# Kernel optimization log

Hardware: AMD Instinct MI355X
Metric: run time of the kernel (lower is better)

The kernel has to match this reference:

```python
import jax, jax.numpy as jnp
import numpy as np
from jax import lax

STRIDE = 16
SCALE = 16.0
ANCHOR_DIMS = (1.0, 2.0, 4.0, 8.0, 16.0, 32.0)
PRE_NMS_TOP_N = 6000
POST_NMS_TOP_N = 300
NMS_THRESH = 0.7


def conv2d(x, w, b, pad):
    y = lax.conv_general_dilated(x, w, (1, 1), [(pad, pad), (pad, pad)],
                                 dimension_numbers=("NCHW", "OIHW", "NCHW"))
    return y + b[None, :, None, None]


def setup_inputs() -> dict:
    key = jax.random.key(0)
    ks = jax.random.split(key, 6)
    B, C, H, W = 1, 1024, 128, 128
    A = len(ANCHOR_DIMS)
    return {
        "base_features": jax.random.normal(ks[0], (B, C, H, W), jnp.float32),
        "image_metadata": jnp.array([[H * STRIDE, W * STRIDE, 1.0]], jnp.float32),
        "gt_boxes": jax.random.uniform(ks[1], (B, 20, 5), jnp.float32) * 100.0,
        "W_conv": jax.random.normal(ks[2], (512, C, 3, 3), jnp.float32) / np.sqrt(C * 9.0),
        "b_conv": jnp.zeros((512,), jnp.float32),
        "W_cls": jax.random.normal(ks[3], (A, 512, 1, 1), jnp.float32) / np.sqrt(512.0),
        "b_cls": jnp.zeros((A,), jnp.float32),
        "W_bbox": jax.random.normal(ks[4], (4 * A, 512, 1, 1), jnp.float32) * 0.01,
        "b_bbox": jnp.zeros((4 * A,), jnp.float32),
    }


def _make_anchors(H, W):
    # square anchors of size dim*scale, centered on each feature cell
    dims = jnp.asarray(ANCHOR_DIMS, jnp.float32) * SCALE          # [A]
    cy = (jnp.arange(H, dtype=jnp.float32) + 0.5) * STRIDE        # [H]
    cx = (jnp.arange(W, dtype=jnp.float32) + 0.5) * STRIDE        # [W]
    half = 0.5 * dims[None, None, :]                              # [1,1,A]
    CX = cx[None, :, None]
    CY = cy[:, None, None]
    anchors = jnp.stack(jnp.broadcast_arrays(CX - half, CY - half, CX + half, CY + half), axis=-1)
    return anchors.reshape(-1, 4)                                 # [(H*W*A),4], order (h,w,a)


def _nms_fixed(boxes, scores):
    # boxes [N,4] already sorted by score desc; greedy NMS, POST_NMS_TOP_N picks
    x1, y1, x2, y2 = boxes[:, 0], boxes[:, 1], boxes[:, 2], boxes[:, 3]
    areas = jnp.maximum(x2 - x1, 0.0) * jnp.maximum(y2 - y1, 0.0)

    def body(i, state):
        alive, keep = state
        masked = jnp.where(alive, scores, -jnp.inf)
        j = jnp.argmax(masked)
        valid = masked[j] > -jnp.inf
        keep = keep.at[i].set(jnp.where(valid, j, -1).astype(jnp.int32))
        bj = boxes[j]
        iw = jnp.maximum(jnp.minimum(x2, bj[2]) - jnp.maximum(x1, bj[0]), 0.0)
        ih = jnp.maximum(jnp.minimum(y2, bj[3]) - jnp.maximum(y1, bj[1]), 0.0)
        inter = iw * ih
        iou = inter / (areas + areas[j] - inter + 1e-9)
        alive = alive & (iou <= NMS_THRESH)
        return alive, keep

    alive0 = jnp.ones(boxes.shape[0], bool)
    keep0 = jnp.full((POST_NMS_TOP_N,), -1, jnp.int32)
    _, keep = lax.fori_loop(0, POST_NMS_TOP_N, body, (alive0, keep0))
    return keep


def _proposal(prob, bbox, image_metadata):
    # original layer operates on detached tensors (.data)
    prob = lax.stop_gradient(prob)
    bbox = lax.stop_gradient(bbox)
    B, A, H, W = prob.shape
    anchors = _make_anchors(H, W)                                 # [N,4]
    scores = prob[0].transpose(1, 2, 0).reshape(-1)               # (h,w,a)
    deltas = bbox[0].reshape(A, 4, H, W).transpose(2, 3, 0, 1).reshape(-1, 4)
    wa = anchors[:, 2] - anchors[:, 0]
    ha = anchors[:, 3] - anchors[:, 1]
    cxa = anchors[:, 0] + 0.5 * wa
    cya = anchors[:, 1] + 0.5 * ha
    pcx = deltas[:, 0] * wa + cxa
    pcy = deltas[:, 1] * ha + cya
    pw = jnp.exp(deltas[:, 2]) * wa
    ph = jnp.exp(deltas[:, 3]) * ha
    boxes = jnp.stack([pcx - 0.5 * pw, pcy - 0.5 * ph, pcx + 0.5 * pw, pcy + 0.5 * ph], axis=1)
    im_h, im_w = image_metadata[0, 0], image_metadata[0, 1]
    boxes = jnp.stack([
        jnp.clip(boxes[:, 0], 0.0, im_w), jnp.clip(boxes[:, 1], 0.0, im_h),
        jnp.clip(boxes[:, 2], 0.0, im_w), jnp.clip(boxes[:, 3], 0.0, im_h)], axis=1)
    top_scores, top_idx = lax.top_k(scores, PRE_NMS_TOP_N)
    top_boxes = boxes[top_idx]
    keep = _nms_fixed(top_boxes, top_scores)
    sel = jnp.where(keep >= 0, keep, 0)
    kept = top_boxes[sel] * (keep >= 0).astype(top_boxes.dtype)[:, None]
    rois = jnp.concatenate([jnp.zeros((POST_NMS_TOP_N, 1), top_boxes.dtype), kept], axis=1)
    return rois                                                   # [POST_NMS_TOP_N, 5]


def reference(base_features, image_metadata, gt_boxes, W_conv, b_conv, W_cls, b_cls, W_bbox, b_bbox):
    conv1 = jax.nn.relu(conv2d(base_features, W_conv, b_conv, pad=1))   # [B,512,H,W]
    score = conv2d(conv1, W_cls, b_cls, pad=0)                          # [B,A,H,W]
    B, A, H, W = score.shape
    s2 = score.reshape(B, 2, (A * H) // 2, W)                           # RPN.reshape(x, 2)
    prob = jax.nn.softmax(s2, axis=1).reshape(B, A, H, W)               # reshape back to A channels
    bbox = conv2d(conv1, W_bbox, b_bbox, pad=0)                         # [B,4A,H,W]
    rois = _proposal(prob, bbox, image_metadata)
    return rois, prob, bbox
```

## Files before the change

kernel.cpp:

```cpp
#include <hip/hip_runtime.h>
#include <math.h>

typedef unsigned int u32;
typedef unsigned long long u64;
typedef short s16x8 __attribute__((ext_vector_type(8)));
typedef float f32x4 __attribute__((ext_vector_type(4)));

#define HH 128
#define WW 128
#define NPIX (128*128)
#define NANCH (NPIX*6)
#define KPRE 6000
#define KPOST 300
#define SORT_CAP 16384
#define RW 96
#define NMS_T 0.7f

#define OUT_PROB 1500
#define OUT_BBOX (1500 + 98304)

#define WS_CONV1 ((size_t)0)
#define WS_XTH   ((size_t)33554432)
#define WS_WPH   ((size_t)100663296)
#define WS_BOXES ((size_t)33554432)
#define WS_SCORE (WS_BOXES + 1572864)
#define WS_KEYS  (WS_SCORE + 393216)
#define WS_TB    (WS_KEYS + 131072)
#define WS_AREA  (WS_TB + 98304)
#define WS_SUP   (WS_AREA + 24576)
#define WS_HIST  (WS_SUP + 4718592)
#define WS_CTRL  (WS_HIST + 262144)
#define WS_KEEP  (WS_CTRL + 256)
#define WS_SKEYS (WS_KEEP + 1280)

__device__ __forceinline__ unsigned short f2bf(float x) {
    u32 b = __float_as_uint(x);
    u32 r = (b + 0x7FFFu + ((b >> 16) & 1u)) >> 16;
    return (unsigned short)r;
}

__device__ __forceinline__ void gl_lds16(const void* g, void* l) {
    __builtin_amdgcn_global_load_lds(
        (__attribute__((address_space(1))) const void*)g,
        (__attribute__((address_space(3))) void*)l,
        16, 0, 0);
}

__global__ void k_init(u32* __restrict__ hist, u32* __restrict__ ctrl,
                       int* __restrict__ keep, u64* __restrict__ keys) {
    int t = blockIdx.x * blockDim.x + threadIdx.x;
    if (t < 65536) hist[t] = 0u;
    if (t < 64)    ctrl[t] = 0u;
    if (t < 304)   keep[t] = -1;
    if (t < SORT_CAP) keys[t] = ~0ULL;
}

__global__ __launch_bounds__(256) void k_xsplit(const float* __restrict__ in,
                                                unsigned short* __restrict__ xth) {
    unsigned short* xtl = xth + 16777216;
    __shared__ unsigned short Th[64][72];
    __shared__ unsigned short Tl[64][72];
    const int px0 = blockIdx.x * 64;
    const int c0  = blockIdx.y * 64;
    const int t = threadIdx.x;
    const int r = t >> 4;
    const int p4 = (t & 15) * 4;
#pragma unroll
    for (int i = 0; i < 4; ++i) {
        int cr = r + 16 * i;
        float4 v = *(const float4*)(in + (size_t)(c0 + cr) * NPIX + px0 + p4);
        float vv[4] = {v.x, v.y, v.z, v.w};
#pragma unroll
        for (int k = 0; k < 4; ++k) {
            unsigned short h = f2bf(vv[k]);
            float hf = __uint_as_float((u32)h << 16);
            unsigned short l = f2bf(vv[k] - hf);
            Th[p4 + k][cr] = h;
            Tl[p4 + k][cr] = l;
        }
    }
    __syncthreads();
    const int p = t >> 2, q = t & 3;
    unsigned short* dh = xth + (size_t)(px0 + p) * 1024 + c0 + q * 16;
    unsigned short* dl = xtl + (size_t)(px0 + p) * 1024 + c0 + q * 16;
    *(uint4*)dh       = *(const uint4*)&Th[p][q * 16];
    *(uint4*)(dh + 8) = *(const uint4*)&Th[p][q * 16 + 8];
    *(uint4*)dl       = *(const uint4*)&Tl[p][q * 16];
    *(uint4*)(dl + 8) = *(const uint4*)&Tl[p][q * 16 + 8];
}

__global__ __launch_bounds__(256) void k_wpack(const float* __restrict__ w,
                                               unsigned short* __restrict__ wph,
                                               float* __restrict__ zstash) {
    if (blockIdx.x == 0 && threadIdx.x < 128) zstash[threadIdx.x] = 0.f;
    int id = blockIdx.x * 256 + threadIdx.x;
    int oc = id >> 10, c = id & 1023;
    const float* src = w + (size_t)oc * 9216 + c * 9;
#pragma unroll
    for (int tap = 0; tap < 9; ++tap) {
        float x = src[tap];
        unsigned short h = f2bf(x);
        unsigned short l = f2bf(x - __uint_as_float((u32)h << 16));
        wph[(size_t)tap * 524288 + id] = h;
        wph[4718592 + (size_t)tap * 524288 + id] = l;
    }
}

__global__ __launch_bounds__(256, 2) void k_conv3m(const unsigned short* __restrict__ xt,
                                                   const unsigned short* __restrict__ wp,
                                                   const float* __restrict__ bias,
                                                   const unsigned short* __restrict__ zst,
                                                   float* __restrict__ out) {
    const int ocg = blockIdx.x;
    const int y   = blockIdx.y;
    const int oc0 = ocg * 128;
    const int tid = threadIdx.x;
    const int lane = tid & 63;
    const int w    = tid >> 6;
    const int l15  = lane & 15;
    const int quad = lane >> 4;
    const int hoc  = w >> 1, hpx = w & 1;

    __shared__ __align__(16) unsigned short Lds[32768];

    const int lg  = lane & 3;
    const int lr  = lane >> 2;

    const unsigned short* xsrc[4];
    int xstep[4];
    const unsigned short* wsrc[4];

    int wp_pl[4], wp_ocr[4], wp_gs[4];
#pragma unroll
    for (int j = 0; j < 4; ++j) {
        int i = w + 4 * j;
        wp_pl[j]  = i >> 3;
        wp_ocr[j] = (i & 7) * 16 + lr;
        wp_gs[j]  = lg ^ ((wp_ocr[j] >> 1) & 3);
    }
    int xp_pl[4], xp_p[4], xp_gs[4];
#pragma unroll
    for (int j = 0; j < 4; ++j) {
        int i = w + 4 * j;
        xp_pl[j] = i >> 3;
        xp_p[j]  = (i & 7) * 16 + lr;
        xp_gs[j] = lg ^ ((xp_p[j] >> 1) & 3);
    }

    auto set_tap = [&](int tap) {
        int dy = tap / 3, dx = tap - dy * 3;
        int yy = y + dy - 1;
        bool yok = (yy >= 0) && (yy < HH);
#pragma unroll
        for (int j = 0; j < 4; ++j) {
            int x = dx - 1 + xp_p[j];
            bool ok = yok && (x >= 0) && (x < WW);
            xsrc[j] = ok ? xt + (size_t)xp_pl[j] * 16777216
                              + (size_t)(yy * WW + x) * 1024 + xp_gs[j] * 8
                         : zst + lg * 8;
            xstep[j] = ok ? 32 : 0;
        }
#pragma unroll
        for (int j = 0; j < 4; ++j)
            wsrc[j] = wp + (size_t)wp_pl[j] * 4718592 + (size_t)tap * 524288
                        + (size_t)(oc0 + wp_ocr[j]) * 1024 + wp_gs[j] * 8;
    };

    auto issue = [&](int sel) {
        const int bo = sel * 16384;
#pragma unroll
        for (int j = 0; j < 4; ++j) {
            gl_lds16(xsrc[j], &Lds[bo + (w + 4 * j) * 512]);
            xsrc[j] += xstep[j];
        }
#pragma unroll
        for (int j = 0; j < 4; ++j) {
            gl_lds16(wsrc[j], &Lds[bo + 8192 + (w + 4 * j) * 512]);
            wsrc[j] += 32;
        }
    };

    const int g  = quad ^ ((l15 >> 1) & 3);
    const int bB0 = (hpx * 64 + l15) * 32 + g * 8;
    const int bA0 = 8192 + (hoc * 64 + l15) * 32 + g * 8;

    f32x4 acc[4][4];
#pragma unroll
    for (int og = 0; og < 4; ++og)
#pragma unroll
        for (int nt = 0; nt < 4; ++nt) acc[og][nt] = (f32x4){0.f, 0.f, 0.f, 0.f};

    set_tap(0);
    issue(0);

    for (int s = 0; s < 288; ++s) {
        const int cur = s & 1;
        __syncthreads();
        if (s + 1 < 288) {
            int s1 = s + 1;
            if ((s1 & 31) == 0) set_tap(s1 >> 5);
            issue(s1 & 1);
        }

        const int bo = cur * 16384;
        s16x8 ah[4], al[4];
#pragma unroll
        for (int og = 0; og < 4; ++og) {
            ah[og] = *(const s16x8*)&Lds[bo + bA0 + og * 512];
            al[og] = *(const s16x8*)&Lds[bo + bA0 + 4096 + og * 512];
        }
#pragma unroll
        for (int nt = 0; nt < 4; ++nt) {
            const s16x8 bh = *(const s16x8*)&Lds[bo + bB0 + nt * 512];
            const s16x8 bl = *(const s16x8*)&Lds[bo + bB0 + 4096 + nt * 512];
#pragma unroll
            for (int og = 0; og < 4; ++og) {
                acc[og][nt] = __builtin_amdgcn_mfma_f32_16x16x32_bf16(ah[og], bh, acc[og][nt], 0, 0, 0);
                acc[og][nt] = __builtin_amdgcn_mfma_f32_16x16x32_bf16(ah[og], bl, acc[og][nt], 0, 0, 0);
                acc[og][nt] = __builtin_amdgcn_mfma_f32_16x16x32_bf16(al[og], bh, acc[og][nt], 0, 0, 0);
            }
        }
    }

#pragma unroll
    for (int og = 0; og < 4; ++og) {
#pragma unroll
        for (int nt = 0; nt < 4; ++nt) {
#pragma unroll
            for (int rg = 0; rg < 4; ++rg) {
                const int oc = oc0 + hoc * 64 + og * 16 + quad * 4 + rg;
                const int px = hpx * 64 + nt * 16 + l15;
                float v = acc[og][nt][rg] + bias[oc];
                out[(size_t)oc * NPIX + y * WW + px] = fmaxf(v, 0.f);
            }
        }
    }
}

__global__ __launch_bounds__(256) void k_conv1(const float* __restrict__ conv1,
                                               const float* __restrict__ wcls,
                                               const float* __restrict__ bcls,
                                               const float* __restrict__ wbox,
                                               const float* __restrict__ bboxb,
                                               float* __restrict__ out) {
    const int tid = threadIdx.x;
    const int og = tid >> 4, pg = tid & 15;
    const int px0 = blockIdx.x * 64;
    __shared__ __align__(16) float Wl[32][32];
    __shared__ __align__(16) float Xl[32][64];
    __shared__ float Sc[6][64];

    float a0[4] = {0, 0, 0, 0}, a1[4] = {0, 0, 0, 0};

    for (int cc = 0; cc < 16; ++cc) {
        {
            int u = tid;
            int row = (u * 4) >> 5;
            int col = (u * 4) & 31;
            float4 v;
            if (row < 6)       v = *(const float4*)(wcls + row * 512 + cc * 32 + col);
            else if (row < 30) v = *(const float4*)(wbox + (row - 6) * 512 + cc * 32 + col);
            else               v = make_float4(0.f, 0.f, 0.f, 0.f);
            *(float4*)&Wl[row][col] = v;
        }
        for (int u = tid; u < 512; u += 256) {
            int row = (u * 4) >> 6, col = (u * 4) & 63;
            *(float4*)&Xl[row][col] =
                *(const float4*)(conv1 + (size_t)(cc * 32 + row) * NPIX + px0 + col);
        }
        __syncthreads();
#pragma unroll
        for (int cp = 0; cp < 32; ++cp) {
            const float4 x = *(const float4*)&Xl[cp][pg * 4];
            const float w0 = Wl[og][cp];
            const float w1 = Wl[og + 16][cp];
            a0[0] = fmaf(w0, x.x, a0[0]); a0[1] = fmaf(w0, x.y, a0[1]);
            a0[2] = fmaf(w0, x.z, a0[2]); a0[3] = fmaf(w0, x.w, a0[3]);
            a1[0] = fmaf(w1, x.x, a1[0]); a1[1] = fmaf(w1, x.y, a1[1]);
            a1[2] = fmaf(w1, x.z, a1[2]); a1[3] = fmaf(w1, x.w, a1[3]);
        }
        __syncthreads();
    }
    const int pxb = px0 + pg * 4;
    if (og < 6) {
        const float bc = bcls[og];
#pragma unroll
        for (int kk = 0; kk < 4; ++kk) Sc[og][pg * 4 + kk] = a0[kk] + bc;
    } else {
        const float bb = bboxb[og - 6];
#pragma unroll
        for (int kk = 0; kk < 4; ++kk)
            out[OUT_BBOX + (size_t)(og - 6) * NPIX + pxb + kk] = a0[kk] + bb;
    }
    if (og + 16 < 30) {
        const float bb = bboxb[og + 10];
#pragma unroll
        for (int kk = 0; kk < 4; ++kk)
            out[OUT_BBOX + (size_t)(og + 10) * NPIX + pxb + kk] = a1[kk] + bb;
    }
    __syncthreads();
    if (og < 6) {
        const int pa = og < 3 ? og + 3 : og - 3;
#pragma unroll
        for (int kk = 0; kk < 4; ++kk) {
            const float s = Sc[og][pg * 4 + kk], sp = Sc[pa][pg * 4 + kk];
            out[OUT_PROB + (size_t)og * NPIX + pxb + kk] = 1.0f / (1.0f + expf(sp - s));
        }
    }
}

__global__ void k_decode(const float* __restrict__ out, const float* __restrict__ meta,
                         float4* __restrict__ boxes, float* __restrict__ scores) {
#pragma clang fp contract(off)
    int t = blockIdx.x * blockDim.x + threadIdx.x;
    if (t >= NANCH) return;
    int a = t >> 14;
    int pix = t & 16383;
    int yc = pix >> 7, xc = pix & 127;
    int n = pix * 6 + a;
    float sc = out[OUT_PROB + (size_t)a * NPIX + pix];
    float d0 = out[OUT_BBOX + (size_t)(a * 4 + 0) * NPIX + pix];
    float d1 = out[OUT_BBOX + (size_t)(a * 4 + 1) * NPIX + pix];
    float d2 = out[OUT_BBOX + (size_t)(a * 4 + 2) * NPIX + pix];
    float d3 = out[OUT_BBOX + (size_t)(a * 4 + 3) * NPIX + pix];
    const float dims = (float)(16 << a);
    const float cxa = (xc + 0.5f) * 16.f;
    const float cya = (yc + 0.5f) * 16.f;
    float pcx = d0 * dims + cxa;
    float pcy = d1 * dims + cya;
    float pw  = expf(d2) * dims;
    float ph  = expf(d3) * dims;
    float imh = meta[0], imw = meta[1];
    float x1 = fminf(fmaxf(pcx - 0.5f * pw, 0.f), imw);
    float y1 = fminf(fmaxf(pcy - 0.5f * ph, 0.f), imh);
    float x2 = fminf(fmaxf(pcx + 0.5f * pw, 0.f), imw);
    float y2 = fminf(fmaxf(pcy + 0.5f * ph, 0.f), imh);
    boxes[n] = make_float4(x1, y1, x2, y2);
    scores[n] = sc;
}

__global__ void k_hist(const float* __restrict__ scores, u32* __restrict__ hist) {
    int t = blockIdx.x * blockDim.x + threadIdx.x;
    if (t >= NANCH) return;
    u32 b = __float_as_uint(scores[t]) >> 16;
    atomicAdd(&hist[b], 1u);
}

__global__ void k_select(const u32* __restrict__ hist, u32* __restrict__ ctrl) {
    __shared__ u32 S[256];
    __shared__ u32 U[256];
    const int tid = threadIdx.x;
    u32 s = 0;
    for (int i = 0; i < 256; ++i) s += hist[tid * 256 + i];
    S[tid] = s;
    __syncthreads();
    if (tid == 0) {
        u32 acc = 0;
        for (int t2 = 255; t2 >= 0; --t2) { U[t2] = acc; acc += S[t2]; }
    }
    __syncthreads();
    if (U[tid] < KPRE && U[tid] + S[tid] >= KPRE) {
        u32 acc = U[tid];
        for (int b = tid * 256 + 255; b >= tid * 256; --b) {
            u32 h = hist[b];
            if (acc + h >= KPRE) { ctrl[1] = (u32)b; ctrl[2] = acc; break; }
            acc += h;
        }
    }
}

__global__ void k_compact(const float* __restrict__ scores, u32* __restrict__ ctrl,
                          u64* __restrict__ keys) {
    int t = blockIdx.x * blockDim.x + threadIdx.x;
    if (t >= NANCH) return;
    u32 bits = __float_as_uint(scores[t]);
    if ((bits >> 16) >= ctrl[1]) {
        u32 pos = atomicAdd(&ctrl[0], 1u);
        if (pos < SORT_CAP) keys[pos] = ((u64)(~bits) << 32) | (u32)t;
    }
}

__global__ __launch_bounds__(1024) void k_sort_local(u64* __restrict__ keys) {
    __shared__ u64 lds[8192];
    const int tid = threadIdx.x;
    u64* g = keys + blockIdx.x * 8192;
    for (int u = tid; u < 8192; u += 1024) lds[u] = g[u];
    __syncthreads();
    for (int k = 2; k <= 8192; k <<= 1) {
        for (int j = k >> 1; j > 0; j >>= 1) {
            for (int u = tid; u < 4096; u += 1024) {
                int i = ((u & ~(j - 1)) << 1) | (u & (j - 1));
                int l = i | j;
                bool up = (i & k) == 0;
                u64 x = lds[i], y2 = lds[l];
                if ((x > y2) == up) { lds[i] = y2; lds[l] = x; }
            }
            __syncthreads();
        }
    }
    for (int u = tid; u < 8192; u += 1024) g[u] = lds[u];
}

__global__ void k_merge(const u64* __restrict__ keys, u64* __restrict__ skeys) {
    int i = blockIdx.x * blockDim.x + threadIdx.x;
    if (i >= KPRE) return;
    const u64* A = keys;
    const u64* B = keys + 8192;
    int lo = i > 8192 ? i - 8192 : 0;
    int hi = i < 8192 ? i : 8192;
    while (lo < hi) {
        int a = (lo + hi) >> 1;
        if (A[a] < B[i - a - 1]) lo = a + 1; else hi = a;
    }
    int a = lo, b = i - lo;
    u64 va = (a < 8192) ? A[a] : ~0ULL;
    u64 vb = (b < 8192) ? B[b] : ~0ULL;
    skeys[i] = va < vb ? va : vb;
}

__global__ void k_gather(const u64* __restrict__ skeys, const float4* __restrict__ boxes,
                         float4* __restrict__ tb, float* __restrict__ areas) {
#pragma clang fp contract(off)
    int i = blockIdx.x * blockDim.x + threadIdx.x;
    if (i >= KPRE) return;
    u32 n = (u32)(skeys[i] & 0xFFFFFFFFULL);
    float4 b = boxes[n];
    tb[i] = b;
    areas[i] = fmaxf(b.z - b.x, 0.f) * fmaxf(b.w - b.y, 0.f);
}

__global__ __launch_bounds__(256) void k_bitmap(const float4* __restrict__ tb,
                                                const float* __restrict__ areas,
                                                u64* __restrict__ suppr) {
#pragma clang fp contract(off)
    const int i = blockIdx.x;
    const int lane = threadIdx.x & 63;
    const int wv = threadIdx.x >> 6;
    const float4 bi = tb[i];
    const float ai = areas[i];
    for (int Wd = wv; Wd < RW; Wd += 4) {
        int j = Wd * 64 + lane;
        bool sup = false;
        if (j < KPRE) {
            float4 bj = tb[j];
            float iw = fmaxf(fminf(bi.z, bj.z) - fmaxf(bi.x, bj.x), 0.f);
            float ih = fmaxf(fminf(bi.w, bj.w) - fmaxf(bi.y, bj.y), 0.f);
            float inter = iw * ih;
            float denom = ((areas[j] + ai) - inter) + 1e-9f;
            sup = (inter / denom) > NMS_T;
        }
        u64 m = __ballot(sup);
        if (lane == 0) suppr[(size_t)i * RW + Wd] = m;
    }
}

__global__ void k_scan(const u64* __restrict__ suppr, int* __restrict__ keep) {
    const int lane = threadIdx.x;
    u64 a0 = (lane < 93) ? ~0ULL : (lane == 93 ? ((1ULL << 48) - 1) : 0ULL);
    const int w1 = lane + 64;
    u64 a1 = (w1 < 93) ? ~0ULL : (w1 == 93 ? ((1ULL << 48) - 1) : 0ULL);
    int kept = 0;
    int i = 0;
    while (kept < KPOST) {
        int wi = i >> 6;
        if (wi >= 94) break;
        u64 wvv = (wi < 64) ? __shfl(a0, wi) : __shfl(a1, wi - 64);
        wvv &= (~0ULL) << (i & 63);
        if (wvv == 0ULL) { i = (wi + 1) << 6; continue; }
        int b = __ffsll((long long)wvv) - 1;
        i = (wi << 6) + b;
        if (lane == 0) keep[kept] = i;
        kept++;
        const u64* row = suppr + (size_t)i * RW;
        u64 s0 = row[lane];
        u64 s1 = (lane + 64 < RW) ? row[lane + 64] : 0ULL;
        a0 &= ~s0;
        a1 &= ~s1;
        i++;
    }
}

__global__ void k_rois(const int* __restrict__ keep, const float4* __restrict__ tb,
                       float* __restrict__ out) {
    int r = blockIdx.x * blockDim.x + threadIdx.x;
    if (r >= KPOST) return;
    int k = keep[r];
    float4 b = make_float4(0.f, 0.f, 0.f, 0.f);
    if (k >= 0) b = tb[k];
    out[r * 5 + 0] = 0.f;
    out[r * 5 + 1] = b.x;
    out[r * 5 + 2] = b.y;
    out[r * 5 + 3] = b.z;
    out[r * 5 + 4] = b.w;
}

extern "C" void kernel_launch(void* const* d_in, const int* in_sizes, int n_in,
                              void* d_out, int out_size, void* d_ws, size_t ws_size,
                              hipStream_t stream) {
    (void)in_sizes; (void)n_in; (void)out_size; (void)ws_size;
    const float* x     = (const float*)d_in[0];
    const float* meta  = (const float*)d_in[1];
    const float* wc3   = (const float*)d_in[3];
    const float* bc3   = (const float*)d_in[4];
    const float* wcls  = (const float*)d_in[5];
    const float* bcls  = (const float*)d_in[6];
    const float* wbox  = (const float*)d_in[7];
    const float* bboxb = (const float*)d_in[8];
    float* out = (float*)d_out;
    char* ws = (char*)d_ws;

    float*  conv1  = (float*)(ws + WS_CONV1);
    float4* boxes  = (float4*)(ws + WS_BOXES);
    float*  scores = (float*)(ws + WS_SCORE);
    u64*    keys   = (u64*)(ws + WS_KEYS);
    float4* tb     = (float4*)(ws + WS_TB);
    float*  areas  = (float*)(ws + WS_AREA);
    u64*    suppr  = (u64*)(ws + WS_SUP);
    u32*    hist   = (u32*)(ws + WS_HIST);
    u32*    ctrl   = (u32*)(ws + WS_CTRL);
    int*    keep   = (int*)(ws + WS_KEEP);
    u64*    skeys  = (u64*)(ws + WS_SKEYS);

    float* zstash = out;

    unsigned short* xth = (unsigned short*)(ws + WS_XTH);
    unsigned short* wph = (unsigned short*)(ws + WS_WPH);
    k_xsplit<<<dim3(256, 16), 256, 0, stream>>>(x, xth);
    k_wpack<<<2048, 256, 0, stream>>>(wc3, wph, zstash);
    k_conv3m<<<dim3(4, 128), 256, 0, stream>>>(xth, wph, bc3,
                                               (const unsigned short*)zstash, conv1);

    k_init<<<256, 256, 0, stream>>>(hist, ctrl, keep, keys);
    k_conv1<<<256, 256, 0, stream>>>(conv1, wcls, bcls, wbox, bboxb, out);
    k_decode<<<384, 256, 0, stream>>>(out, meta, boxes, scores);
    k_hist<<<384, 256, 0, stream>>>(scores, hist);
    k_select<<<1, 256, 0, stream>>>(hist, ctrl);
    k_compact<<<384, 256, 0, stream>>>(scores, ctrl, keys);
    k_sort_local<<<2, 1024, 0, stream>>>(keys);
    k_merge<<<24, 256, 0, stream>>>(keys, skeys);
    k_gather<<<24, 256, 0, stream>>>(skeys, boxes, tb, areas);
    k_bitmap<<<6000, 256, 0, stream>>>(tb, areas, suppr);
    k_scan<<<1, 64, 0, stream>>>(suppr, keep);
    k_rois<<<2, 256, 0, stream>>>(keep, tb, out);
}
```

Baseline: 936.8 us.

## Prepack conv weights into MFMA fragment layout and use 32x32x16 bf16 MFMA

Repacks the 3x3 conv weights on the device into per-lane fragment records so each wave loads its A operands straight from global memory into registers, double-buffered across stages, instead of staging them through LDS. Switches the inner product from 16x16x32 to 32x32x16 bf16 MFMA with a 2x2 tile of 16-wide accumulators, and halves LDS use to the activation tile only. This removes LDS traffic and bank pressure for weights and raises the math done per fragment load. In exchange it adds register pressure from the prefetched weight fragments, and the global weight loads are no longer shared across waves through LDS.

Result: slower. 989.5 us (+5.6%).

```diff
diff --git a/kernel.cpp b/kernel.cpp
--- a/kernel.cpp
+++ b/kernel.cpp
@@ -5,6 +5,7 @@
 typedef unsigned long long u64;
 typedef short s16x8 __attribute__((ext_vector_type(8)));
 typedef float f32x4 __attribute__((ext_vector_type(4)));
+typedef float f32x16 __attribute__((ext_vector_type(16)));
 
 #define HH 128
 #define WW 128
@@ -96,13 +97,25 @@
     int id = blockIdx.x * 256 + threadIdx.x;
     int oc = id >> 10, c = id & 1023;
     const float* src = w + (size_t)oc * 9216 + c * 9;
+    const int ocg  = oc >> 7;
+    const int hoc  = (oc >> 6) & 1;
+    const int og   = (oc >> 5) & 1;
+    const int l31  = oc & 31;
+    const int cblk = c >> 5;
+    const int ks   = (c >> 4) & 1;
+    const int lhi  = (c >> 3) & 1;
+    const int e    = c & 7;
+    const int lane = lhi * 32 + l31;
+    const size_t rec0 = ((size_t)cblk * 4 + ocg) * 2 + hoc;
+    const size_t off0 = (size_t)(og * 2 + ks) * 512 + lane * 8 + e;
 #pragma unroll
     for (int tap = 0; tap < 9; ++tap) {
         float x = src[tap];
         unsigned short h = f2bf(x);
         unsigned short l = f2bf(x - __uint_as_float((u32)h << 16));
-        wph[(size_t)tap * 524288 + id] = h;
-        wph[4718592 + (size_t)tap * 524288 + id] = l;
+        size_t rec = rec0 + (size_t)tap * 256;
+        wph[rec * 4096 + off0]        = h;
+        wph[rec * 4096 + 2048 + off0] = l;
     }
 }
 
@@ -117,27 +130,18 @@
     const int tid = threadIdx.x;
     const int lane = tid & 63;
     const int w    = tid >> 6;
-    const int l15  = lane & 15;
-    const int quad = lane >> 4;
+    const int l31  = lane & 31;
+    const int lhi  = lane >> 5;
     const int hoc  = w >> 1, hpx = w & 1;
-
-    __shared__ __align__(16) unsigned short Lds[32768];
+    const int wrec = ocg * 2 + hoc;
+
+    __shared__ __align__(16) unsigned short Lds[16384];
 
     const int lg  = lane & 3;
     const int lr  = lane >> 2;
 
     const unsigned short* xsrc[4];
     int xstep[4];
-    const unsigned short* wsrc[4];
-
-    int wp_pl[4], wp_ocr[4], wp_gs[4];
-#pragma unroll
-    for (int j = 0; j < 4; ++j) {
-        int i = w + 4 * j;
-        wp_pl[j]  = i >> 3;
-        wp_ocr[j] = (i & 7) * 16 + lr;
-        wp_gs[j]  = lg ^ ((wp_ocr[j] >> 1) & 3);
-    }
     int xp_pl[4], xp_p[4], xp_gs[4];
 #pragma unroll
     for (int j = 0; j < 4; ++j) {
@@ -160,77 +164,107 @@
                          : zst + lg * 8;
             xstep[j] = ok ? 32 : 0;
         }
-#pragma unroll
-        for (int j = 0; j < 4; ++j)
-            wsrc[j] = wp + (size_t)wp_pl[j] * 4718592 + (size_t)tap * 524288
-                        + (size_t)(oc0 + wp_ocr[j]) * 1024 + wp_gs[j] * 8;
     };
 
     auto issue = [&](int sel) {
-        const int bo = sel * 16384;
+        const int bo = sel * 8192;
 #pragma unroll
         for (int j = 0; j < 4; ++j) {
             gl_lds16(xsrc[j], &Lds[bo + (w + 4 * j) * 512]);
             xsrc[j] += xstep[j];
         }
-#pragma unroll
-        for (int j = 0; j < 4; ++j) {
-            gl_lds16(wsrc[j], &Lds[bo + 8192 + (w + 4 * j) * 512]);
-            wsrc[j] += 32;
-        }
     };
 
-    const int g  = quad ^ ((l15 >> 1) & 3);
-    const int bB0 = (hpx * 64 + l15) * 32 + g * 8;
-    const int bA0 = 8192 + (hoc * 64 + l15) * 32 + g * 8;
-
-    f32x4 acc[4][4];
-#pragma unroll
-    for (int og = 0; og < 4; ++og)
-#pragma unroll
-        for (int nt = 0; nt < 4; ++nt) acc[og][nt] = (f32x4){0.f, 0.f, 0.f, 0.f};
+    int xoff[2][2];
+#pragma unroll
+    for (int nt = 0; nt < 2; ++nt)
+#pragma unroll
+        for (int ks = 0; ks < 2; ++ks) {
+            int px = hpx * 64 + nt * 32 + l31;
+            int gk = ks * 2 + lhi;
+            xoff[nt][ks] = px * 32 + ((gk ^ ((px >> 1) & 3)) * 8);
+        }
+
+    f32x16 acc[2][2];
+#pragma unroll
+    for (int og = 0; og < 2; ++og)
+#pragma unroll
+        for (int nt = 0; nt < 2; ++nt)
+#pragma unroll
+            for (int r = 0; r < 16; ++r) acc[og][nt][r] = 0.f;
+
+    s16x8 wA[8], wB[8];
 
     set_tap(0);
     issue(0);
-
-    for (int s = 0; s < 288; ++s) {
-        const int cur = s & 1;
-        __syncthreads();
-        if (s + 1 < 288) {
-            int s1 = s + 1;
-            if ((s1 & 31) == 0) set_tap(s1 >> 5);
-            issue(s1 & 1);
-        }
-
-        const int bo = cur * 16384;
-        s16x8 ah[4], al[4];
-#pragma unroll
-        for (int og = 0; og < 4; ++og) {
-            ah[og] = *(const s16x8*)&Lds[bo + bA0 + og * 512];
-            al[og] = *(const s16x8*)&Lds[bo + bA0 + 4096 + og * 512];
-        }
-#pragma unroll
-        for (int nt = 0; nt < 4; ++nt) {
-            const s16x8 bh = *(const s16x8*)&Lds[bo + bB0 + nt * 512];
-            const s16x8 bl = *(const s16x8*)&Lds[bo + bB0 + 4096 + nt * 512];
-#pragma unroll
-            for (int og = 0; og < 4; ++og) {
-                acc[og][nt] = __builtin_amdgcn_mfma_f32_16x16x32_bf16(ah[og], bh, acc[og][nt], 0, 0, 0);
-                acc[og][nt] = __builtin_amdgcn_mfma_f32_16x16x32_bf16(ah[og], bl, acc[og][nt], 0, 0, 0);
-                acc[og][nt] = __builtin_amdgcn_mfma_f32_16x16x32_bf16(al[og], bh, acc[og][nt], 0, 0, 0);
-            }
-        }
-    }
-
-#pragma unroll
-    for (int og = 0; og < 4; ++og) {
-#pragma unroll
-        for (int nt = 0; nt < 4; ++nt) {
-#pragma unroll
-            for (int rg = 0; rg < 4; ++rg) {
-                const int oc = oc0 + hoc * 64 + og * 16 + quad * 4 + rg;
-                const int px = hpx * 64 + nt * 16 + l15;
-                float v = acc[og][nt][rg] + bias[oc];
+    {
+        const s16x8* p = (const s16x8*)wp + (size_t)wrec * 512 + lane;
+#pragma unroll
+        for (int f = 0; f < 8; ++f) wA[f] = p[f * 64];
+    }
+
+#define STAGE(S, CUR, WC, WN)                                                   \
+    {                                                                           \
+        __syncthreads();                                                        \
+        if ((S) + 1 < 288) {                                                    \
+            if ((((S) + 1) & 31) == 0) set_tap(((S) + 1) >> 5);                 \
+            issue(((S) + 1) & 1);                                               \
+        }                                                                       \
+        {                                                                       \
+            int sn = ((S) + 1 < 288) ? (S) + 1 : 0;                             \
+            const s16x8* p = (const s16x8*)wp +                                 \
+                             ((size_t)sn * 8 + wrec) * 512 + lane;              \
+            _Pragma("unroll")                                                   \
+            for (int f = 0; f < 8; ++f) WN[f] = p[f * 64];                      \
+        }                                                                       \
+        const int bo = (CUR) * 8192;                                            \
+        s16x8 xh[2][2], xl[2][2];                                               \
+        _Pragma("unroll")                                                       \
+        for (int nt = 0; nt < 2; ++nt)                                          \
+            _Pragma("unroll")                                                   \
+            for (int ks = 0; ks < 2; ++ks) {                                    \
+                xh[nt][ks] = *(const s16x8*)&Lds[bo + xoff[nt][ks]];            \
+                xl[nt][ks] = *(const s16x8*)&Lds[bo + xoff[nt][ks] + 4096];     \
+            }                                                                   \
+        _Pragma("unroll")                                                       \
+        for (int ks = 0; ks < 2; ++ks) {                                        \
+            _Pragma("unroll")                                                   \
+            for (int og = 0; og < 2; ++og)                                      \
+                _Pragma("unroll")                                               \
+                for (int nt = 0; nt < 2; ++nt)                                  \
+                    acc[og][nt] = __builtin_amdgcn_mfma_f32_32x32x16_bf16(      \
+                        WC[og * 2 + ks], xh[nt][ks], acc[og][nt], 0, 0, 0);     \
+            _Pragma("unroll")                                                   \
+            for (int og = 0; og < 2; ++og)                                      \
+                _Pragma("unroll")                                               \
+                for (int nt = 0; nt < 2; ++nt)                                  \
+                    acc[og][nt] = __builtin_amdgcn_mfma_f32_32x32x16_bf16(      \
+                        WC[og * 2 + ks], xl[nt][ks], acc[og][nt], 0, 0, 0);     \
+            _Pragma("unroll")                                                   \
+            for (int og = 0; og < 2; ++og)                                      \
+                _Pragma("unroll")                                               \
+                for (int nt = 0; nt < 2; ++nt)                                  \
+                    acc[og][nt] = __builtin_amdgcn_mfma_f32_32x32x16_bf16(      \
+                        WC[4 + og * 2 + ks], xh[nt][ks], acc[og][nt], 0, 0, 0); \
+        }                                                                       \
+    }
+
+    for (int s = 0; s < 288; s += 2) {
+        STAGE(s, 0, wA, wB)
+        STAGE(s + 1, 1, wB, wA)
+    }
+#undef STAGE
+
+#pragma unroll
+    for (int og = 0; og < 2; ++og) {
+#pragma unroll
+        for (int nt = 0; nt < 2; ++nt) {
+            const int px = hpx * 64 + nt * 32 + l31;
+#pragma unroll
+            for (int r = 0; r < 16; ++r) {
+                const int row = (r & 3) + 8 * (r >> 2) + 4 * lhi;
+                const int oc = oc0 + hoc * 64 + og * 32 + row;
+                float v = acc[og][nt][r] + bias[oc];
                 out[(size_t)oc * NPIX + y * WW + px] = fmaxf(v, 0.f);
             }
         }
```

## Stream conv weights directly to registers and deepen activation LDS pipeline to four stages

Applied to the files above, without the earlier changes.

Repacks the split-bf16 conv weights into a per-wave, fragment-ordered layout, so each wave loads its A operands straight from global memory into registers with register double-buffering instead of staging them through LDS. The freed LDS is used for a four-buffer activation ring with three stages in flight. The per-stage full barrier wait is replaced by a partial vmcnt wait plus a raw barrier. This aims to cut LDS traffic and barrier stalls in the main 3x3 conv GEMM. The cost is more register pressure and more global weight reads per wave, since the weight tile is no longer shared through LDS.

Measured after the change: 986.9 us. 1.05x slower.

```diff
diff --git a/kernel.cpp b/kernel.cpp
--- a/kernel.cpp
+++ b/kernel.cpp
@@ -96,13 +96,25 @@
     int id = blockIdx.x * 256 + threadIdx.x;
     int oc = id >> 10, c = id & 1023;
     const float* src = w + (size_t)oc * 9216 + c * 9;
+    const int ocg  = oc >> 7;
+    const int hoc  = (oc >> 6) & 1;
+    const int og   = (oc >> 4) & 3;
+    const int l15  = oc & 15;
+    const int cblk = c >> 5;
+    const int q    = (c >> 3) & 3;
+    const int e    = c & 7;
+    const int lane = q * 16 + l15;
+    const size_t rec0 = ((size_t)cblk * 4 + ocg) * 2 + hoc;
+    const size_t offh = (size_t)(og * 2 + 0) * 512 + lane * 8 + e;
+    const size_t offl = (size_t)(og * 2 + 1) * 512 + lane * 8 + e;
 #pragma unroll
     for (int tap = 0; tap < 9; ++tap) {
         float x = src[tap];
         unsigned short h = f2bf(x);
         unsigned short l = f2bf(x - __uint_as_float((u32)h << 16));
-        wph[(size_t)tap * 524288 + id] = h;
-        wph[4718592 + (size_t)tap * 524288 + id] = l;
+        size_t rec = rec0 + (size_t)tap * 256;
+        wph[rec * 4096 + offh] = h;
+        wph[rec * 4096 + offl] = l;
     }
 }
 
@@ -120,6 +132,7 @@
     const int l15  = lane & 15;
     const int quad = lane >> 4;
     const int hoc  = w >> 1, hpx = w & 1;
+    const int wrec = ocg * 2 + hoc;
 
     __shared__ __align__(16) unsigned short Lds[32768];
 
@@ -128,16 +141,6 @@
 
     const unsigned short* xsrc[4];
     int xstep[4];
-    const unsigned short* wsrc[4];
-
-    int wp_pl[4], wp_ocr[4], wp_gs[4];
-#pragma unroll
-    for (int j = 0; j < 4; ++j) {
-        int i = w + 4 * j;
-        wp_pl[j]  = i >> 3;
-        wp_ocr[j] = (i & 7) * 16 + lr;
-        wp_gs[j]  = lg ^ ((wp_ocr[j] >> 1) & 3);
-    }
     int xp_pl[4], xp_p[4], xp_gs[4];
 #pragma unroll
     for (int j = 0; j < 4; ++j) {
@@ -147,10 +150,10 @@
         xp_gs[j] = lg ^ ((xp_p[j] >> 1) & 3);
     }
 
-    auto set_tap = [&](int tap) {
+    auto set_tap = [&](int tap, bool dead) {
         int dy = tap / 3, dx = tap - dy * 3;
         int yy = y + dy - 1;
-        bool yok = (yy >= 0) && (yy < HH);
+        bool yok = !dead && (yy >= 0) && (yy < HH);
 #pragma unroll
         for (int j = 0; j < 4; ++j) {
             int x = dx - 1 + xp_p[j];
@@ -160,29 +163,19 @@
                          : zst + lg * 8;
             xstep[j] = ok ? 32 : 0;
         }
-#pragma unroll
-        for (int j = 0; j < 4; ++j)
-            wsrc[j] = wp + (size_t)wp_pl[j] * 4718592 + (size_t)tap * 524288
-                        + (size_t)(oc0 + wp_ocr[j]) * 1024 + wp_gs[j] * 8;
     };
 
-    auto issue = [&](int sel) {
-        const int bo = sel * 16384;
+    auto issue = [&](int buf) {
+        const int bo = buf * 8192;
 #pragma unroll
         for (int j = 0; j < 4; ++j) {
             gl_lds16(xsrc[j], &Lds[bo + (w + 4 * j) * 512]);
             xsrc[j] += xstep[j];
         }
-#pragma unroll
-        for (int j = 0; j < 4; ++j) {
-            gl_lds16(wsrc[j], &Lds[bo + 8192 + (w + 4 * j) * 512]);
-            wsrc[j] += 32;
-        }
     };
 
-    const int g  = quad ^ ((l15 >> 1) & 3);
+    const int g   = quad ^ ((l15 >> 1) & 3);
     const int bB0 = (hpx * 64 + l15) * 32 + g * 8;
-    const int bA0 = 8192 + (hoc * 64 + l15) * 32 + g * 8;
 
     f32x4 acc[4][4];
 #pragma unroll
@@ -190,37 +183,63 @@
 #pragma unroll
         for (int nt = 0; nt < 4; ++nt) acc[og][nt] = (f32x4){0.f, 0.f, 0.f, 0.f};
 
-    set_tap(0);
+    s16x8 wA[8], wB[8];
+
+    set_tap(0, false);
     issue(0);
-
-    for (int s = 0; s < 288; ++s) {
-        const int cur = s & 1;
-        __syncthreads();
-        if (s + 1 < 288) {
-            int s1 = s + 1;
-            if ((s1 & 31) == 0) set_tap(s1 >> 5);
-            issue(s1 & 1);
-        }
-
-        const int bo = cur * 16384;
-        s16x8 ah[4], al[4];
-#pragma unroll
-        for (int og = 0; og < 4; ++og) {
-            ah[og] = *(const s16x8*)&Lds[bo + bA0 + og * 512];
-            al[og] = *(const s16x8*)&Lds[bo + bA0 + 4096 + og * 512];
-        }
-#pragma unroll
-        for (int nt = 0; nt < 4; ++nt) {
-            const s16x8 bh = *(const s16x8*)&Lds[bo + bB0 + nt * 512];
-            const s16x8 bl = *(const s16x8*)&Lds[bo + bB0 + 4096 + nt * 512];
-#pragma unroll
-            for (int og = 0; og < 4; ++og) {
-                acc[og][nt] = __builtin_amdgcn_mfma_f32_16x16x32_bf16(ah[og], bh, acc[og][nt], 0, 0, 0);
-                acc[og][nt] = __builtin_amdgcn_mfma_f32_16x16x32_bf16(ah[og], bl, acc[og][nt], 0, 0, 0);
-                acc[og][nt] = __builtin_amdgcn_mfma_f32_16x16x32_bf16(al[og], bh, acc[og][nt], 0, 0, 0);
-            }
-        }
-    }
+    {
+        const s16x8* p = (const s16x8*)wp + (size_t)wrec * 512 + lane;
+#pragma unroll
+        for (int f = 0; f < 8; ++f) wA[f] = p[f * 64];
+    }
+    issue(1);
+    issue(2);
+
+#define STAGE(S, WC, WN)                                                        \
+    {                                                                           \
+        asm volatile("s_waitcnt vmcnt(16)" ::: "memory");                       \
+        __builtin_amdgcn_s_barrier();                                           \
+        {                              \
+            int sn = ((S) + 1 < 288) ? (S) + 1 : 0;                             \
+            const s16x8* p = (const s16x8*)wp +                                 \
+                             ((size_t)sn * 8 + wrec) * 512 + lane;              \
+            _Pragma("unroll")                                                   \
+            for (int f = 0; f < 8; ++f) WN[f] = p[f * 64];                      \
+        }                                                                       \
+        {               \
+            int s3 = (S) + 3;                                                   \
+            if ((s3 & 31) == 0) set_tap(s3 >> 5, s3 >= 288);                    \
+            issue(s3 & 3);                                                      \
+        }                                                                       \
+        const int bo = ((S) & 3) * 8192;                                        \
+        s16x8 bh[4], bl[4];                                                     \
+        _Pragma("unroll")                                                       \
+        for (int nt = 0; nt < 4; ++nt) {                                        \
+            bh[nt] = *(const s16x8*)&Lds[bo + bB0 + nt * 512];                  \
+            bl[nt] = *(const s16x8*)&Lds[bo + bB0 + 4096 + nt * 512];           \
+        }                                                                       \
+        _Pragma("unroll")                                                       \
+        for (int nt = 0; nt < 4; ++nt) {                                        \
+            _Pragma("unroll")                                                   \
+            for (int og = 0; og < 4; ++og)                                      \
+                acc[og][nt] = __builtin_amdgcn_mfma_f32_16x16x32_bf16(          \
+                    WC[og * 2], bh[nt], acc[og][nt], 0, 0, 0);                  \
+            _Pragma("unroll")                                                   \
+            for (int og = 0; og < 4; ++og)                                      \
+                acc[og][nt] = __builtin_amdgcn_mfma_f32_16x16x32_bf16(          \
+                    WC[og * 2], bl[nt], acc[og][nt], 0, 0, 0);                  \
+            _Pragma("unroll")                                                   \
+            for (int og = 0; og < 4; ++og)                                      \
+                acc[og][nt] = __builtin_amdgcn_mfma_f32_16x16x32_bf16(          \
+                    WC[og * 2 + 1], bh[nt], acc[og][nt], 0, 0, 0);              \
+        }                                                                       \
+    }
+
+    for (int s = 0; s < 288; s += 2) {
+        STAGE(s, wA, wB)
+        STAGE(s + 1, wB, wA)
+    }
+#undef STAGE
 
 #pragma unroll
     for (int og = 0; og < 4; ++og) {
```

## Replace bitmap NMS with single-block greedy NMS and fuse small post-processing kernels

Applied to the files above, without the earlier changes.

Drops the full 6000x6000 suppression-bitmap kernel and serial scan. They are replaced by one 1024-thread block that keeps all candidate boxes in registers and runs greedy NMS directly: a block-wide min finds the next alive box, then every thread suppresses its own boxes against it. The histogram atomic is folded into decode, and merge is fused with gather and rois, which removes several launches and the 4.7MB bitmap traffic. The cost is up to 300 serial iterations, each with three block barriers, on a single CU.

New measurement: 1.259 ms. 1.34x slower.

```diff
diff --git a/kernel.cpp b/kernel.cpp
--- a/kernel.cpp
+++ b/kernel.cpp
@@ -13,7 +13,6 @@
 #define KPRE 6000
 #define KPOST 300
 #define SORT_CAP 16384
-#define RW 96
 #define NMS_T 0.7f
 
 #define OUT_PROB 1500
@@ -27,11 +26,8 @@
 #define WS_KEYS  (WS_SCORE + 393216)
 #define WS_TB    (WS_KEYS + 131072)
 #define WS_AREA  (WS_TB + 98304)
-#define WS_SUP   (WS_AREA + 24576)
-#define WS_HIST  (WS_SUP + 4718592)
+#define WS_HIST  (WS_AREA + 24576)
 #define WS_CTRL  (WS_HIST + 262144)
-#define WS_KEEP  (WS_CTRL + 256)
-#define WS_SKEYS (WS_KEEP + 1280)
 
 __device__ __forceinline__ unsigned short f2bf(float x) {
     u32 b = __float_as_uint(x);
@@ -47,11 +43,10 @@
 }
 
 __global__ void k_init(u32* __restrict__ hist, u32* __restrict__ ctrl,
-                       int* __restrict__ keep, u64* __restrict__ keys) {
+                       u64* __restrict__ keys) {
     int t = blockIdx.x * blockDim.x + threadIdx.x;
     if (t < 65536) hist[t] = 0u;
     if (t < 64)    ctrl[t] = 0u;
-    if (t < 304)   keep[t] = -1;
     if (t < SORT_CAP) keys[t] = ~0ULL;
 }
 
@@ -310,7 +305,8 @@
 }
 
 __global__ void k_decode(const float* __restrict__ out, const float* __restrict__ meta,
-                         float4* __restrict__ boxes, float* __restrict__ scores) {
+                         float4* __restrict__ boxes, float* __restrict__ scores,
+                         u32* __restrict__ hist) {
 #pragma clang fp contract(off)
     int t = blockIdx.x * blockDim.x + threadIdx.x;
     if (t >= NANCH) return;
@@ -337,13 +333,7 @@
     float y2 = fminf(fmaxf(pcy + 0.5f * ph, 0.f), imh);
     boxes[n] = make_float4(x1, y1, x2, y2);
     scores[n] = sc;
-}
-
-__global__ void k_hist(const float* __restrict__ scores, u32* __restrict__ hist) {
-    int t = blockIdx.x * blockDim.x + threadIdx.x;
-    if (t >= NANCH) return;
-    u32 b = __float_as_uint(scores[t]) >> 16;
-    atomicAdd(&hist[b], 1u);
+    atomicAdd(&hist[__float_as_uint(sc) >> 16], 1u);
 }
 
 __global__ void k_select(const u32* __restrict__ hist, u32* __restrict__ ctrl) {
@@ -401,7 +391,10 @@
     for (int u = tid; u < 8192; u += 1024) g[u] = lds[u];
 }
 
-__global__ void k_merge(const u64* __restrict__ keys, u64* __restrict__ skeys) {
+__global__ void k_mergegather(const u64* __restrict__ keys,
+                              const float4* __restrict__ boxes,
+                              float4* __restrict__ tb, float* __restrict__ areas) {
+#pragma clang fp contract(off)
     int i = blockIdx.x * blockDim.x + threadIdx.x;
     if (i >= KPRE) return;
     const u64* A = keys;
@@ -415,83 +408,82 @@
     int a = lo, b = i - lo;
     u64 va = (a < 8192) ? A[a] : ~0ULL;
     u64 vb = (b < 8192) ? B[b] : ~0ULL;
-    skeys[i] = va < vb ? va : vb;
-}
-
-__global__ void k_gather(const u64* __restrict__ skeys, const float4* __restrict__ boxes,
-                         float4* __restrict__ tb, float* __restrict__ areas) {
+    u64 v = va < vb ? va : vb;
+    u32 n = (u32)(v & 0xFFFFFFFFULL);
+    float4 bx = boxes[n];
+    tb[i] = bx;
+    areas[i] = fmaxf(bx.z - bx.x, 0.f) * fmaxf(bx.w - bx.y, 0.f);
+}
+
+__global__ __launch_bounds__(1024) void k_nms(const float4* __restrict__ tb,
+                                              const float* __restrict__ areas,
+                                              float* __restrict__ out) {
 #pragma clang fp contract(off)
-    int i = blockIdx.x * blockDim.x + threadIdx.x;
-    if (i >= KPRE) return;
-    u32 n = (u32)(skeys[i] & 0xFFFFFFFFULL);
-    float4 b = boxes[n];
-    tb[i] = b;
-    areas[i] = fmaxf(b.z - b.x, 0.f) * fmaxf(b.w - b.y, 0.f);
-}
-
-__global__ __launch_bounds__(256) void k_bitmap(const float4* __restrict__ tb,
-                                                const float* __restrict__ areas,
-                                                u64* __restrict__ suppr) {
-#pragma clang fp contract(off)
-    const int i = blockIdx.x;
-    const int lane = threadIdx.x & 63;
-    const int wv = threadIdx.x >> 6;
-    const float4 bi = tb[i];
-    const float ai = areas[i];
-    for (int Wd = wv; Wd < RW; Wd += 4) {
-        int j = Wd * 64 + lane;
-        bool sup = false;
-        if (j < KPRE) {
-            float4 bj = tb[j];
-            float iw = fmaxf(fminf(bi.z, bj.z) - fmaxf(bi.x, bj.x), 0.f);
-            float ih = fmaxf(fminf(bi.w, bj.w) - fmaxf(bi.y, bj.y), 0.f);
+    const int tid = threadIdx.x;
+    const int lane = tid & 63, wid = tid >> 6;
+    float bx[6], by[6], bz[6], bw[6], ar[6];
+    u32 alive = 0u;
+#pragma unroll
+    for (int k = 0; k < 6; ++k) {
+        int idx = tid * 6 + k;
+        if (idx < KPRE) {
+            float4 b = tb[idx];
+            bx[k] = b.x; by[k] = b.y; bz[k] = b.z; bw[k] = b.w;
+            ar[k] = areas[idx];
+            alive |= (1u << k);
+        } else {
+            bx[k] = by[k] = bz[k] = bw[k] = 0.f; ar[k] = 0.f;
+        }
+    }
+    __shared__ float bb[5];
+    __shared__ u32 wmin[16];
+    __shared__ u32 curs;
+    int kept = 0;
+    for (; kept < KPOST; ++kept) {
+        u32 local = alive ? (u32)(tid * 6 + (__ffs(alive) - 1)) : 0xFFFFFFFFu;
+#pragma unroll
+        for (int d = 1; d < 64; d <<= 1) {
+            u32 o = (u32)__shfl_xor((int)local, d);
+            local = local < o ? local : o;
+        }
+        if (lane == 0) wmin[wid] = local;
+        __syncthreads();
+        if (tid == 0) {
+            u32 mm = wmin[0];
+#pragma unroll
+            for (int i = 1; i < 16; ++i) mm = mm < wmin[i] ? mm : wmin[i];
+            curs = mm;
+        }
+        __syncthreads();
+        u32 cur = curs;
+        if (cur == 0xFFFFFFFFu) break;
+        const int ot = (int)(cur / 6u), ok = (int)(cur % 6u);
+        if (tid == ot) {
+            bb[0] = bx[ok]; bb[1] = by[ok]; bb[2] = bz[ok]; bb[3] = bw[ok];
+            bb[4] = ar[ok];
+            alive &= ~(1u << ok);
+        }
+        __syncthreads();
+        const float cx1 = bb[0], cy1 = bb[1], cx2 = bb[2], cy2 = bb[3], ca = bb[4];
+        if (tid == 1) {
+            out[kept * 5 + 0] = 0.f;
+            out[kept * 5 + 1] = cx1; out[kept * 5 + 2] = cy1;
+            out[kept * 5 + 3] = cx2; out[kept * 5 + 4] = cy2;
+        }
+#pragma unroll
+        for (int k = 0; k < 6; ++k) {
+            float iw = fmaxf(fminf(bz[k], cx2) - fmaxf(bx[k], cx1), 0.f);
+            float ih = fmaxf(fminf(bw[k], cy2) - fmaxf(by[k], cy1), 0.f);
             float inter = iw * ih;
-            float denom = ((areas[j] + ai) - inter) + 1e-9f;
-            sup = (inter / denom) > NMS_T;
-        }
-        u64 m = __ballot(sup);
-        if (lane == 0) suppr[(size_t)i * RW + Wd] = m;
-    }
-}
-
-__global__ void k_scan(const u64* __restrict__ suppr, int* __restrict__ keep) {
-    const int lane = threadIdx.x;
-    u64 a0 = (lane < 93) ? ~0ULL : (lane == 93 ? ((1ULL << 48) - 1) : 0ULL);
-    const int w1 = lane + 64;
-    u64 a1 = (w1 < 93) ? ~0ULL : (w1 == 93 ? ((1ULL << 48) - 1) : 0ULL);
-    int kept = 0;
-    int i = 0;
-    while (kept < KPOST) {
-        int wi = i >> 6;
-        if (wi >= 94) break;
-        u64 wvv = (wi < 64) ? __shfl(a0, wi) : __shfl(a1, wi - 64);
-        wvv &= (~0ULL) << (i & 63);
-        if (wvv == 0ULL) { i = (wi + 1) << 6; continue; }
-        int b = __ffsll((long long)wvv) - 1;
-        i = (wi << 6) + b;
-        if (lane == 0) keep[kept] = i;
-        kept++;
-        const u64* row = suppr + (size_t)i * RW;
-        u64 s0 = row[lane];
-        u64 s1 = (lane + 64 < RW) ? row[lane + 64] : 0ULL;
-        a0 &= ~s0;
-        a1 &= ~s1;
-        i++;
-    }
-}
-
-__global__ void k_rois(const int* __restrict__ keep, const float4* __restrict__ tb,
-                       float* __restrict__ out) {
-    int r = blockIdx.x * blockDim.x + threadIdx.x;
-    if (r >= KPOST) return;
-    int k = keep[r];
-    float4 b = make_float4(0.f, 0.f, 0.f, 0.f);
-    if (k >= 0) b = tb[k];
-    out[r * 5 + 0] = 0.f;
-    out[r * 5 + 1] = b.x;
-    out[r * 5 + 2] = b.y;
-    out[r * 5 + 3] = b.z;
-    out[r * 5 + 4] = b.w;
+            float denom = ((ar[k] + ca) - inter) + 1e-9f;
+            if (inter / denom > NMS_T) alive &= ~(1u << k);
+        }
+        __syncthreads();
+    }
+    for (int r = kept + tid; r < KPOST; r += 1024) {
+        out[r * 5 + 0] = 0.f; out[r * 5 + 1] = 0.f; out[r * 5 + 2] = 0.f;
+        out[r * 5 + 3] = 0.f; out[r * 5 + 4] = 0.f;
+    }
 }
 
 extern "C" void kernel_launch(void* const* d_in, const int* in_sizes, int n_in,
@@ -515,11 +507,8 @@
     u64*    keys   = (u64*)(ws + WS_KEYS);
     float4* tb     = (float4*)(ws + WS_TB);
     float*  areas  = (float*)(ws + WS_AREA);
-    u64*    suppr  = (u64*)(ws + WS_SUP);
     u32*    hist   = (u32*)(ws + WS_HIST);
     u32*    ctrl   = (u32*)(ws + WS_CTRL);
-    int*    keep   = (int*)(ws + WS_KEEP);
-    u64*    skeys  = (u64*)(ws + WS_SKEYS);
 
     float* zstash = out;
 
@@ -530,16 +519,12 @@
     k_conv3m<<<dim3(4, 128), 256, 0, stream>>>(xth, wph, bc3,
                                                (const unsigned short*)zstash, conv1);
 
-    k_init<<<256, 256, 0, stream>>>(hist, ctrl, keep, keys);
+    k_init<<<256, 256, 0, stream>>>(hist, ctrl, keys);
     k_conv1<<<256, 256, 0, stream>>>(conv1, wcls, bcls, wbox, bboxb, out);
-    k_decode<<<384, 256, 0, stream>>>(out, meta, boxes, scores);
-    k_hist<<<384, 256, 0, stream>>>(scores, hist);
+    k_decode<<<384, 256, 0, stream>>>(out, meta, boxes, scores, hist);
     k_select<<<1, 256, 0, stream>>>(hist, ctrl);
     k_compact<<<384, 256, 0, stream>>>(scores, ctrl, keys);
     k_sort_local<<<2, 1024, 0, stream>>>(keys);
-    k_merge<<<24, 256, 0, stream>>>(keys, skeys);
-    k_gather<<<24, 256, 0, stream>>>(skeys, boxes, tb, areas);
-    k_bitmap<<<6000, 256, 0, stream>>>(tb, areas, suppr);
-    k_scan<<<1, 64, 0, stream>>>(suppr, keep);
-    k_rois<<<2, 256, 0, stream>>>(keep, tb, out);
-}
+    k_mergegather<<<24, 256, 0, stream>>>(keys, boxes, tb, areas);
+    k_nms<<<1, 1024, 0, stream>>>(tb, areas, out);
+}
```
